# Kernel optimization log

Hardware: AMD Instinct MI355X
Metric: run time of the kernel (lower is better)

Reference implementation:

```python
import jax, jax.numpy as jnp
import numpy as np

E = 1024      # embed_dim
WS = 64       # window_size
B = 4
S = WS * WS   # residual add only works if seq_len == window_size**2
HID = 4 * E
EPS = 1e-5
SCALE = E ** -0.5


def _layer_norm(x, g, b):
    m = jnp.mean(x, axis=-1, keepdims=True)
    v = jnp.mean(jnp.square(x - m), axis=-1, keepdims=True)
    return (x - m) * jax.lax.rsqrt(v + EPS) * g + b


def setup_inputs() -> dict:
    key = jax.random.key(0)
    ks = jax.random.split(key, 12)
    std = 0.02
    return {
        "x":  jax.random.normal(ks[0], (B, S, E), jnp.float32),
        "Wq": jax.random.normal(ks[1], (E, E), jnp.float32) * std,
        "bq": jnp.zeros((E,), jnp.float32),
        "Wk": jax.random.normal(ks[2], (E, E), jnp.float32) * std,
        "bk": jnp.zeros((E,), jnp.float32),
        "Wv": jax.random.normal(ks[3], (E, E), jnp.float32) * std,
        "bv": jnp.zeros((E,), jnp.float32),
        "g1": jnp.ones((E,), jnp.float32),
        "be1": jnp.zeros((E,), jnp.float32),
        "W1": jax.random.normal(ks[4], (E, HID), jnp.float32) * std,
        "b1": jnp.zeros((HID,), jnp.float32),
        "W2": jax.random.normal(ks[5], (HID, E), jnp.float32) * std,
        "b2": jnp.zeros((E,), jnp.float32),
        "g2": jnp.ones((E,), jnp.float32),
        "be2": jnp.zeros((E,), jnp.float32),
    }


def reference(x, Wq, bq, Wk, bk, Wv, bv, g1, be1, W1, b1, W2, b2, g2, be2):
    b, s, e = x.shape
    n = (b * s) // (WS * WS)
    q = (x @ Wq + bq).reshape(n, WS, WS, e)
    k = (x @ Wk + bk).reshape(n, WS, WS, e)
    v = (x @ Wv + bv).reshape(n, WS, WS, e)
    # per-window attention over the last WS tokens of each (n, w) group
    scores = jnp.einsum('nwqe,nwke->nwqk', q, k) * SCALE  # (n, WS, WS, WS)
    attn = jax.nn.softmax(scores, axis=-1)
    out = jnp.einsum('nwqk,nwke->nwqe', attn, v).reshape(b, s, e)
    x = _layer_norm(x + out, g1, be1)               # dropout is identity (eval)
    ffn = jax.nn.relu(x @ W1 + b1) @ W2 + b2
    x = _layer_norm(x + ffn, g2, be2)
    return x
```

## Files before the change

### kernel.cpp

```cpp
#include <hip/hip_runtime.h>
#include <hip/hip_bf16.h>
#include <stdint.h>


typedef __attribute__((ext_vector_type(4))) float f32x4;
typedef __attribute__((ext_vector_type(8))) short bf16x8;
typedef __attribute__((ext_vector_type(4))) short bf16x4;

__device__ __forceinline__ void async_cp16(const void* g, void* l) {
    __builtin_amdgcn_global_load_lds(
        (const __attribute__((address_space(1))) void*)g,
        (__attribute__((address_space(3))) void*)l,
        16, 0, 0);
}

__device__ __forceinline__ short f2bf(float f) {
    __hip_bfloat16 h = __float2bfloat16(f);
    return __builtin_bit_cast(short, h);
}
__device__ __forceinline__ float bf2f(short s) {
    return __bfloat162float(__builtin_bit_cast(__hip_bfloat16, s));
}

template <int RELU, int MODE>
__global__ __launch_bounds__(512, 2) void gemm256_kernel(
    const short* __restrict__ A, int lda,
    const short* __restrict__ Bt, int ldb,
    const float* __restrict__ bias,
    void* __restrict__ Cv, int ldc,
    int M, int N, int K)
{
    __shared__ __align__(16) short lds[65536];

    const int t = threadIdx.x;
    const int wave = t >> 6, lane = t & 63;
    const int quad = lane >> 4, l16 = lane & 15;
    const int wm = wave >> 2, wn = wave & 3;
    const long m0 = (long)blockIdx.x * 256;
    const long n0 = (long)blockIdx.y * 256;

    const int srow = t >> 2;
    const int sg = t & 3;
    const int lr0 = srow ^ ((srow >> 2) & 1);
    const int lg0 = sg ^ (lr0 & 3);
    const short* gA = A + (m0 + lr0) * (long)lda + lg0 * 8;
    const short* gB = Bt + (n0 + lr0) * (long)ldb + lg0 * 8;
    const int wdst = wave * 512;

    int offA[8], offB[4];
#pragma unroll
    for (int mf = 0; mf < 8; ++mf) {
        const int row = wm * 128 + mf * 16 + l16;
        offA[mf] = (row * 32 + quad * 8) ^ ((row & 7) << 3);
    }
#pragma unroll
    for (int nf = 0; nf < 4; ++nf) {
        const int row = wn * 64 + nf * 16 + l16;
        offB[nf] = (row * 32 + quad * 8) ^ ((row & 7) << 3);
    }

    f32x4 acc[8][4] = {};
    const int NT = K >> 6;

#define STAGE_A(ksub, kt, buf)                                                 \
    do {                                                                       \
        const int ko_ = (kt) * 64 + (ksub) * 32;                               \
        short* d_ = lds + (buf) * 32768 + (ksub) * 8192 + wdst;                \
        async_cp16(gA + ko_, d_);                                              \
        async_cp16(gA + 128 * (long)lda + ko_, d_ + 4096);                     \
    } while (0)
#define STAGE_B(ksub, kt, buf)                                                 \
    do {                                                                       \
        const int ko_ = (kt) * 64 + (ksub) * 32;                               \
        short* d_ = lds + (buf) * 32768 + 16384 + (ksub) * 8192 + wdst;        \
        async_cp16(gB + ko_, d_);                                              \
        async_cp16(gB + 128 * (long)ldb + ko_, d_ + 4096);                     \
    } while (0)

    STAGE_A(0, 0, 0); STAGE_B(0, 0, 0); STAGE_A(1, 0, 0); STAGE_B(1, 0, 0);
    asm volatile("s_waitcnt vmcnt(4)" ::: "memory");
    __builtin_amdgcn_s_barrier();

    for (int kt = 0; kt < NT; ++kt) {
        const int cbuf = kt & 1, nbuf = cbuf ^ 1;
        const short* Ab = lds + cbuf * 32768;
        const short* Bb = Ab + 16384;
        const bool more = (kt + 1 < NT);

        bf16x8 av[4], bv[4];

#pragma unroll
        for (int nf = 0; nf < 4; ++nf) bv[nf] = *(const bf16x8*)(Bb + offB[nf]);
#pragma unroll
        for (int i = 0; i < 4; ++i) av[i] = *(const bf16x8*)(Ab + offA[i]);
        if (more) STAGE_A(0, kt + 1, nbuf);
        __builtin_amdgcn_s_barrier();
        asm volatile("s_waitcnt lgkmcnt(0)" ::: "memory");
        __builtin_amdgcn_sched_barrier(0);
        __builtin_amdgcn_s_setprio(1);
#pragma unroll
        for (int i = 0; i < 4; ++i)
#pragma unroll
            for (int nf = 0; nf < 4; ++nf)
                acc[i][nf] = __builtin_amdgcn_mfma_f32_16x16x32_bf16(
                    av[i], bv[nf], acc[i][nf], 0, 0, 0);
        __builtin_amdgcn_s_setprio(0);
        __builtin_amdgcn_s_barrier();

#pragma unroll
        for (int i = 0; i < 4; ++i) av[i] = *(const bf16x8*)(Ab + offA[4 + i]);
        if (more) STAGE_B(0, kt + 1, nbuf);
        __builtin_amdgcn_s_barrier();
        asm volatile("s_waitcnt lgkmcnt(0)" ::: "memory");
        __builtin_amdgcn_sched_barrier(0);
        __builtin_amdgcn_s_setprio(1);
#pragma unroll
        for (int i = 0; i < 4; ++i)
#pragma unroll
            for (int nf = 0; nf < 4; ++nf)
                acc[4 + i][nf] = __builtin_amdgcn_mfma_f32_16x16x32_bf16(
                    av[i], bv[nf], acc[4 + i][nf], 0, 0, 0);
        __builtin_amdgcn_s_setprio(0);
        if (more) asm volatile("s_waitcnt vmcnt(4)" ::: "memory");
        else      asm volatile("s_waitcnt vmcnt(0)" ::: "memory");
        __builtin_amdgcn_s_barrier();

#pragma unroll
        for (int nf = 0; nf < 4; ++nf) bv[nf] = *(const bf16x8*)(Bb + 8192 + offB[nf]);
#pragma unroll
        for (int i = 0; i < 4; ++i) av[i] = *(const bf16x8*)(Ab + 8192 + offA[i]);
        if (more) STAGE_A(1, kt + 1, nbuf);
        __builtin_amdgcn_s_barrier();
        asm volatile("s_waitcnt lgkmcnt(0)" ::: "memory");
        __builtin_amdgcn_sched_barrier(0);
        __builtin_amdgcn_s_setprio(1);
#pragma unroll
        for (int i = 0; i < 4; ++i)
#pragma unroll
            for (int nf = 0; nf < 4; ++nf)
                acc[i][nf] = __builtin_amdgcn_mfma_f32_16x16x32_bf16(
                    av[i], bv[nf], acc[i][nf], 0, 0, 0);
        __builtin_amdgcn_s_setprio(0);
        __builtin_amdgcn_s_barrier();

#pragma unroll
        for (int i = 0; i < 4; ++i) av[i] = *(const bf16x8*)(Ab + 8192 + offA[4 + i]);
        if (more) STAGE_B(1, kt + 1, nbuf);
        __builtin_amdgcn_s_barrier();
        asm volatile("s_waitcnt lgkmcnt(0)" ::: "memory");
        __builtin_amdgcn_sched_barrier(0);
        __builtin_amdgcn_s_setprio(1);
#pragma unroll
        for (int i = 0; i < 4; ++i)
#pragma unroll
            for (int nf = 0; nf < 4; ++nf)
                acc[4 + i][nf] = __builtin_amdgcn_mfma_f32_16x16x32_bf16(
                    av[i], bv[nf], acc[4 + i][nf], 0, 0, 0);
        __builtin_amdgcn_s_setprio(0);
        if (more) {
            asm volatile("s_waitcnt vmcnt(4)" ::: "memory");
            __builtin_amdgcn_s_barrier();
        }
    }
#undef STAGE_A
#undef STAGE_B

#pragma unroll
    for (int mf = 0; mf < 8; ++mf) {
#pragma unroll
        for (int nf = 0; nf < 4; ++nf) {
            const int n = (int)n0 + wn * 64 + nf * 16 + l16;
            const float bz = (MODE == 2) ? 0.f : bias[n];
#pragma unroll
            for (int r = 0; r < 4; ++r) {
                const long m = m0 + wm * 128 + mf * 16 + quad * 4 + r;
                float v = acc[mf][nf][r] + bz;
                if (MODE == 0) {
                    if (RELU) v = fmaxf(v, 0.f);
                    ((short*)Cv)[m * ldc + n] = f2bf(v);
                } else if (MODE == 1) {
                    ((float*)Cv)[m * ldc + n] = v;
                } else {
                    ((float*)Cv)[m * ldc + n] += v;
                }
            }
        }
    }
}

__global__ __launch_bounds__(256) void attn_mfma_kernel(
    const short* __restrict__ QKV, short* __restrict__ O)
{
    __shared__ __align__(16) float Sf[64 * 65];
    __shared__ __align__(16) short Pb[64 * 72];
    __shared__ __align__(16) short Vt[256 * 72];

    const int t = threadIdx.x;
    const int wave = t >> 6, lane = t & 63;
    const int quad = lane >> 4, l16 = lane & 15;
    const long rowbase = (long)blockIdx.x * 64;
    const short* Qg = QKV + rowbase * 3072;
    const short* Kg = Qg + 1024;
    const short* Vg = Qg + 2048;

    {
        const int wy = wave >> 1, wx = wave & 1;
        const short* qp0 = Qg + (long)(wy * 32 + l16) * 3072 + quad * 8;
        const short* qp1 = qp0 + 16 * 3072;
        const short* kp0 = Kg + (long)(wx * 32 + l16) * 3072 + quad * 8;
        const short* kp1 = kp0 + 16 * 3072;

        f32x4 s00 = {}, s01 = {}, s10 = {}, s11 = {};
        bf16x8 a0 = *(const bf16x8*)qp0;
        bf16x8 a1 = *(const bf16x8*)qp1;
        bf16x8 b0 = *(const bf16x8*)kp0;
        bf16x8 b1 = *(const bf16x8*)kp1;

#pragma unroll 2
        for (int k0 = 0; k0 < 1024; k0 += 32) {
            const int kn = (k0 + 32 < 1024) ? k0 + 32 : 0;
            bf16x8 na0 = *(const bf16x8*)(qp0 + kn);
            bf16x8 na1 = *(const bf16x8*)(qp1 + kn);
            bf16x8 nb0 = *(const bf16x8*)(kp0 + kn);
            bf16x8 nb1 = *(const bf16x8*)(kp1 + kn);
            s00 = __builtin_amdgcn_mfma_f32_16x16x32_bf16(a0, b0, s00, 0, 0, 0);
            s01 = __builtin_amdgcn_mfma_f32_16x16x32_bf16(a0, b1, s01, 0, 0, 0);
            s10 = __builtin_amdgcn_mfma_f32_16x16x32_bf16(a1, b0, s10, 0, 0, 0);
            s11 = __builtin_amdgcn_mfma_f32_16x16x32_bf16(a1, b1, s11, 0, 0, 0);
            a0 = na0; a1 = na1; b0 = nb0; b1 = nb1;
        }

        const int rb = wy * 32 + quad * 4;
        const int cb = wx * 32 + l16;
#pragma unroll
        for (int r = 0; r < 4; ++r) {
            Sf[(rb + r) * 65 + cb]           = s00[r] * 0.03125f;
            Sf[(rb + r) * 65 + cb + 16]      = s01[r] * 0.03125f;
            Sf[(rb + 16 + r) * 65 + cb]      = s10[r] * 0.03125f;
            Sf[(rb + 16 + r) * 65 + cb + 16] = s11[r] * 0.03125f;
        }
    }
    __syncthreads();

    {
        const int row = t >> 2;
        const int cs = (t & 3) * 16;
        const float* sp = Sf + row * 65 + cs;
        float v[16];
        float mx = -1e30f;
#pragma unroll
        for (int j = 0; j < 16; ++j) { v[j] = sp[j]; mx = fmaxf(mx, v[j]); }
        mx = fmaxf(mx, __shfl_xor(mx, 1, 64));
        mx = fmaxf(mx, __shfl_xor(mx, 2, 64));
        float sum = 0.f;
#pragma unroll
        for (int j = 0; j < 16; ++j) { v[j] = __expf(v[j] - mx); sum += v[j]; }
        sum += __shfl_xor(sum, 1, 64);
        sum += __shfl_xor(sum, 2, 64);
        const float inv = 1.f / sum;
        short* pp = Pb + row * 72 + cs;
        bf16x8 o0, o1;
#pragma unroll
        for (int j = 0; j < 8; ++j) { o0[j] = f2bf(v[j] * inv); o1[j] = f2bf(v[8 + j] * inv); }
        *(bf16x8*)(pp) = o0;
        *(bf16x8*)(pp + 8) = o1;
    }
    __syncthreads();

    bf16x8 am[2][4];
#pragma unroll
    for (int ki = 0; ki < 2; ++ki)
#pragma unroll
        for (int mi = 0; mi < 4; ++mi)
            am[ki][mi] = *(const bf16x8*)(Pb + (mi * 16 + l16) * 72 + ki * 32 + quad * 8);

    for (int nc = 0; nc < 4; ++nc) {
        const int nbase = nc * 256;
#pragma unroll
        for (int it = 0; it < 8; ++it) {
            const int idx = it * 256 + t;
            const int tok = idx >> 5;
            const int grp = idx & 31;
            bf16x8 v = *(const bf16x8*)(Vg + (long)tok * 3072 + nbase + grp * 8);
            const int tsw = tok ^ ((grp & 7) << 3);
            short* dst = Vt + (grp * 8) * 72 + tsw;
#pragma unroll
            for (int j = 0; j < 8; ++j) dst[j * 72] = v[j];
        }
        __syncthreads();

        f32x4 acc[4][4] = {};
#pragma unroll
        for (int ki = 0; ki < 2; ++ki) {
            bf16x8 bn[4];
#pragma unroll
            for (int ni = 0; ni < 4; ++ni) {
                const int e_local = wave * 64 + ni * 16 + l16;
                const int s = (e_local >> 3) & 7;
                bn[ni] = *(const bf16x8*)(Vt + e_local * 72 + ((ki * 32 + quad * 8) ^ (s << 3)));
            }
#pragma unroll
            for (int mi = 0; mi < 4; ++mi)
#pragma unroll
                for (int ni = 0; ni < 4; ++ni)
                    acc[mi][ni] = __builtin_amdgcn_mfma_f32_16x16x32_bf16(
                        am[ki][mi], bn[ni], acc[mi][ni], 0, 0, 0);
        }

#pragma unroll
        for (int mi = 0; mi < 4; ++mi)
#pragma unroll
            for (int ni = 0; ni < 4; ++ni) {
                const long n = nbase + wave * 64 + ni * 16 + l16;
#pragma unroll
                for (int r = 0; r < 4; ++r) {
                    const long m = rowbase + mi * 16 + quad * 4 + r;
                    O[m * 1024 + n] = f2bf(acc[mi][ni][r]);
                }
            }
        __syncthreads();
    }
}

__global__ __launch_bounds__(256, 4) void ln1_kernel(
    const float* __restrict__ X, const short* __restrict__ R,
    const float* __restrict__ gamma, const float* __restrict__ beta,
    short* __restrict__ Y)
{
    __shared__ float red[8];
    const int t = threadIdx.x;
    const int wave = t >> 6, lane = t & 63;
    const long row = blockIdx.x;

    f32x4 xv = *(const f32x4*)(X + row * 1024 + t * 4);
    bf16x4 rv = *(const bf16x4*)(R + row * 1024 + t * 4);
    float v[4];
    float s = 0.f, sq = 0.f;
#pragma unroll
    for (int i = 0; i < 4; ++i) {
        v[i] = xv[i] + bf2f(rv[i]);
        s += v[i];
        sq += v[i] * v[i];
    }
#pragma unroll
    for (int off = 32; off > 0; off >>= 1) {
        s  += __shfl_down(s, off, 64);
        sq += __shfl_down(sq, off, 64);
    }
    if (lane == 0) { red[wave] = s; red[4 + wave] = sq; }
    __syncthreads();
    if (t == 0) {
        float S = red[0] + red[1] + red[2] + red[3];
        float Q = red[4] + red[5] + red[6] + red[7];
        float mean = S * (1.f / 1024.f);
        float var = fmaxf(Q * (1.f / 1024.f) - mean * mean, 0.f);
        red[0] = mean;
        red[1] = rsqrtf(var + 1e-5f);
    }
    __syncthreads();
    const float mean = red[0], rstd = red[1];
    f32x4 gv = *(const f32x4*)(gamma + t * 4);
    f32x4 bv = *(const f32x4*)(beta + t * 4);
    bf16x4 yv;
#pragma unroll
    for (int i = 0; i < 4; ++i)
        yv[i] = f2bf((v[i] - mean) * rstd * gv[i] + bv[i]);
    *(bf16x4*)(Y + row * 1024 + t * 4) = yv;
}

__global__ __launch_bounds__(256, 4) void ln2_kernel(
    const short* __restrict__ X1, float* __restrict__ F,
    const float* __restrict__ gamma, const float* __restrict__ beta)
{
    __shared__ float red[8];
    const int t = threadIdx.x;
    const int wave = t >> 6, lane = t & 63;
    const long row = blockIdx.x;

    bf16x4 xv = *(const bf16x4*)(X1 + row * 1024 + t * 4);
    f32x4 fv = *(const f32x4*)(F + row * 1024 + t * 4);
    float v[4];
    float s = 0.f, sq = 0.f;
#pragma unroll
    for (int i = 0; i < 4; ++i) {
        v[i] = bf2f(xv[i]) + fv[i];
        s += v[i];
        sq += v[i] * v[i];
    }
#pragma unroll
    for (int off = 32; off > 0; off >>= 1) {
        s  += __shfl_down(s, off, 64);
        sq += __shfl_down(sq, off, 64);
    }
    if (lane == 0) { red[wave] = s; red[4 + wave] = sq; }
    __syncthreads();
    if (t == 0) {
        float S = red[0] + red[1] + red[2] + red[3];
        float Q = red[4] + red[5] + red[6] + red[7];
        float mean = S * (1.f / 1024.f);
        float var = fmaxf(Q * (1.f / 1024.f) - mean * mean, 0.f);
        red[0] = mean;
        red[1] = rsqrtf(var + 1e-5f);
    }
    __syncthreads();
    const float mean = red[0], rstd = red[1];
    f32x4 gv = *(const f32x4*)(gamma + t * 4);
    f32x4 bv = *(const f32x4*)(beta + t * 4);
    f32x4 yv;
#pragma unroll
    for (int i = 0; i < 4; ++i)
        yv[i] = (v[i] - mean) * rstd * gv[i] + bv[i];
    *(f32x4*)(F + row * 1024 + t * 4) = yv;
}

__global__ __launch_bounds__(256, 2) void transpose_kernel(
    const float* __restrict__ W, short* __restrict__ WT, int K, int N)
{
    __shared__ __align__(16) short tile[64 * 72];
    const int t = threadIdx.x;
    const long kb = (long)blockIdx.x * 64, nb = (long)blockIdx.y * 64;
    const int r = t >> 3, c = (t & 7) << 3;
#pragma unroll
    for (int i = 0; i < 2; ++i) {
        f32x4 v0 = *(const f32x4*)(W + (kb + r + i * 32) * N + nb + c);
        f32x4 v1 = *(const f32x4*)(W + (kb + r + i * 32) * N + nb + c + 4);
        short* dst = tile + (r + i * 32) * 72 + c;
#pragma unroll
        for (int j = 0; j < 4; ++j) { dst[j] = f2bf(v0[j]); dst[4 + j] = f2bf(v1[j]); }
    }
    __syncthreads();
#pragma unroll
    for (int i = 0; i < 2; ++i) {
        const int rr = r + i * 32;
        bf16x8 o;
#pragma unroll
        for (int j = 0; j < 8; ++j) o[j] = tile[(c + j) * 72 + rr];
        *(bf16x8*)(WT + (nb + rr) * K + kb + c) = o;
    }
}

__global__ __launch_bounds__(256, 4) void cvt_kernel(
    const float* __restrict__ X, short* __restrict__ Y)
{
    const long i = ((long)blockIdx.x * 256 + threadIdx.x) * 4;
    f32x4 v = *(const f32x4*)(X + i);
    bf16x4 o;
#pragma unroll
    for (int j = 0; j < 4; ++j) o[j] = f2bf(v[j]);
    *(bf16x4*)(Y + i) = o;
}

__global__ void concat_bias_kernel(const float* __restrict__ bq,
                                   const float* __restrict__ bk,
                                   const float* __restrict__ bv,
                                   float* __restrict__ out)
{
    const int i = blockIdx.x * 256 + threadIdx.x;
    float v;
    if (i < 1024)      v = bq[i];
    else if (i < 2048) v = bk[i - 1024];
    else               v = bv[i - 2048];
    out[i] = v;
}

extern "C" void kernel_launch(void* const* d_in, const int* in_sizes, int n_in,
                              void* d_out, int out_size, void* d_ws, size_t ws_size,
                              hipStream_t stream)
{
    const float* x   = (const float*)d_in[0];
    const float* Wq  = (const float*)d_in[1];
    const float* bq  = (const float*)d_in[2];
    const float* Wk  = (const float*)d_in[3];
    const float* bk  = (const float*)d_in[4];
    const float* Wv  = (const float*)d_in[5];
    const float* bv  = (const float*)d_in[6];
    const float* g1  = (const float*)d_in[7];
    const float* be1 = (const float*)d_in[8];
    const float* W1  = (const float*)d_in[9];
    const float* b1  = (const float*)d_in[10];
    const float* W2  = (const float*)d_in[11];
    const float* b2  = (const float*)d_in[12];
    const float* g2  = (const float*)d_in[13];
    const float* be2 = (const float*)d_in[14];

    const int M = in_sizes[0] / 1024;
    float* F    = (float*)d_out;
    short* xbf  = (short*)d_out;
    short* Obf  = (short*)d_out + (size_t)M * 1024;

    char* ws = (char*)d_ws;
    short* WqkvT = (short*)ws;
    short* W1T   = (short*)(ws + 6291456);
    short* W2T   = (short*)(ws + 14680064);
    float* bqkv  = (float*)(ws + 23068672);
    short* QKV   = (short*)(ws + 23080960);
    short* Hh    = (short*)(ws + 23080960);
    short* x1    = (short*)(ws + 23080960 + (size_t)M * 2048 * 2);

    dim3 blk(256);
    dim3 blk5(512);
    transpose_kernel<<<dim3(16, 16), blk, 0, stream>>>(Wq, WqkvT,               1024, 1024);
    transpose_kernel<<<dim3(16, 16), blk, 0, stream>>>(Wk, WqkvT + 1024 * 1024, 1024, 1024);
    transpose_kernel<<<dim3(16, 16), blk, 0, stream>>>(Wv, WqkvT + 2048 * 1024, 1024, 1024);
    transpose_kernel<<<dim3(16, 64), blk, 0, stream>>>(W1, W1T, 1024, 4096);
    transpose_kernel<<<dim3(64, 16), blk, 0, stream>>>(W2, W2T, 4096, 1024);
    concat_bias_kernel<<<12, blk, 0, stream>>>(bq, bk, bv, bqkv);
    cvt_kernel<<<M, blk, 0, stream>>>(x, xbf);

    gemm256_kernel<0, 0><<<dim3(M / 256, 12), blk5, 0, stream>>>(
        xbf, 1024, WqkvT, 1024, bqkv, QKV, 3072, M, 3072, 1024);
    attn_mfma_kernel<<<M / 64, blk, 0, stream>>>(QKV, Obf);
    ln1_kernel<<<M, blk, 0, stream>>>(x, Obf, g1, be1, x1);
    gemm256_kernel<1, 0><<<dim3(M / 256, 8), blk5, 0, stream>>>(
        x1, 1024, W1T, 1024, b1, Hh, 2048, M, 2048, 1024);
    gemm256_kernel<0, 1><<<dim3(M / 256, 4), blk5, 0, stream>>>(
        Hh, 2048, W2T, 4096, b2, F, 1024, M, 1024, 2048);
    gemm256_kernel<1, 0><<<dim3(M / 256, 8), blk5, 0, stream>>>(
        x1, 1024, W1T + 2048 * 1024, 1024, b1 + 2048, Hh, 2048, M, 2048, 1024);
    gemm256_kernel<0, 2><<<dim3(M / 256, 4), blk5, 0, stream>>>(
        Hh, 2048, W2T + 2048, 4096, b2, F, 1024, M, 1024, 2048);
    ln2_kernel<<<M, blk, 0, stream>>>(x1, F, g2, be2);
}
```

Baseline: 676.0 us.

## Restructure GEMM main loop into register-prefetched quadrant MFMA schedule

Reorganizes the 256x256 GEMM K-loop. All four global->LDS copies for the next tile are issued at the start of each iteration, and the loop now works over quadrants of the output (A rows 0-3/4-7 crossed with B cols low/high) with both k-subtiles per quadrant. Fragments for the next tile are loaded from LDS into registers before the last MFMA block runs, and partial lgkmcnt waits let LDS reads overlap MFMA execution. The aim is fewer barriers and waits per k-step and more LDS-latency hiding, at the cost of many more live registers (A0/A4/Bl/Bh), which may lower occupancy or cause spills.

```diff
diff --git a/kernel.cpp b/kernel.cpp
--- a/kernel.cpp
+++ b/kernel.cpp
@@ -77,9 +77,23 @@
         async_cp16(gB + 128 * (long)ldb + ko_, d_ + 4096);                     \
     } while (0)
 
+    bf16x8 A0[8], A4[8], Bl[4], Bh[4];
+
     STAGE_A(0, 0, 0); STAGE_B(0, 0, 0); STAGE_A(1, 0, 0); STAGE_B(1, 0, 0);
-    asm volatile("s_waitcnt vmcnt(4)" ::: "memory");
+    asm volatile("s_waitcnt vmcnt(0)" ::: "memory");
     __builtin_amdgcn_s_barrier();
+    {
+        const short* Ab = lds;
+        const short* Bb = lds + 16384;
+#pragma unroll
+        for (int i = 0; i < 4; ++i) A0[i]     = *(const bf16x8*)(Ab + offA[i]);
+#pragma unroll
+        for (int i = 0; i < 4; ++i) A0[4 + i] = *(const bf16x8*)(Ab + 8192 + offA[i]);
+        Bl[0] = *(const bf16x8*)(Bb + offB[0]);
+        Bl[1] = *(const bf16x8*)(Bb + offB[1]);
+        Bl[2] = *(const bf16x8*)(Bb + 8192 + offB[0]);
+        Bl[3] = *(const bf16x8*)(Bb + 8192 + offB[1]);
+    }
 
     for (int kt = 0; kt < NT; ++kt) {
         const int cbuf = kt & 1, nbuf = cbuf ^ 1;
@@ -87,80 +101,85 @@
         const short* Bb = Ab + 16384;
         const bool more = (kt + 1 < NT);
 
-        bf16x8 av[4], bv[4];
-
-#pragma unroll
-        for (int nf = 0; nf < 4; ++nf) bv[nf] = *(const bf16x8*)(Bb + offB[nf]);
-#pragma unroll
-        for (int i = 0; i < 4; ++i) av[i] = *(const bf16x8*)(Ab + offA[i]);
-        if (more) STAGE_A(0, kt + 1, nbuf);
+        if (more) {
+            STAGE_A(0, kt + 1, nbuf); STAGE_B(0, kt + 1, nbuf);
+            STAGE_A(1, kt + 1, nbuf); STAGE_B(1, kt + 1, nbuf);
+        }
+
+        Bh[0] = *(const bf16x8*)(Bb + offB[2]);
+        Bh[1] = *(const bf16x8*)(Bb + offB[3]);
+        Bh[2] = *(const bf16x8*)(Bb + 8192 + offB[2]);
+        Bh[3] = *(const bf16x8*)(Bb + 8192 + offB[3]);
+        asm volatile("s_waitcnt lgkmcnt(4)" ::: "memory");
+        __builtin_amdgcn_sched_barrier(0);
+        __builtin_amdgcn_s_setprio(1);
+#pragma unroll
+        for (int ks = 0; ks < 2; ++ks)
+#pragma unroll
+            for (int mf = 0; mf < 4; ++mf)
+#pragma unroll
+                for (int nf = 0; nf < 2; ++nf)
+                    acc[mf][nf] = __builtin_amdgcn_mfma_f32_16x16x32_bf16(
+                        A0[ks * 4 + mf], Bl[ks * 2 + nf], acc[mf][nf], 0, 0, 0);
+        __builtin_amdgcn_s_setprio(0);
         __builtin_amdgcn_s_barrier();
+
+#pragma unroll
+        for (int i = 0; i < 4; ++i) A4[i]     = *(const bf16x8*)(Ab + offA[4 + i]);
+#pragma unroll
+        for (int i = 0; i < 4; ++i) A4[4 + i] = *(const bf16x8*)(Ab + 8192 + offA[4 + i]);
+        asm volatile("s_waitcnt lgkmcnt(8)" ::: "memory");
+        __builtin_amdgcn_sched_barrier(0);
+        __builtin_amdgcn_s_setprio(1);
+#pragma unroll
+        for (int ks = 0; ks < 2; ++ks)
+#pragma unroll
+            for (int mf = 0; mf < 4; ++mf)
+#pragma unroll
+                for (int nf = 0; nf < 2; ++nf)
+                    acc[mf][2 + nf] = __builtin_amdgcn_mfma_f32_16x16x32_bf16(
+                        A0[ks * 4 + mf], Bh[ks * 2 + nf], acc[mf][2 + nf], 0, 0, 0);
+        __builtin_amdgcn_s_setprio(0);
+        __builtin_amdgcn_s_barrier();
+
         asm volatile("s_waitcnt lgkmcnt(0)" ::: "memory");
         __builtin_amdgcn_sched_barrier(0);
         __builtin_amdgcn_s_setprio(1);
 #pragma unroll
-        for (int i = 0; i < 4; ++i)
-#pragma unroll
-            for (int nf = 0; nf < 4; ++nf)
-                acc[i][nf] = __builtin_amdgcn_mfma_f32_16x16x32_bf16(
-                    av[i], bv[nf], acc[i][nf], 0, 0, 0);
+        for (int ks = 0; ks < 2; ++ks)
+#pragma unroll
+            for (int mf = 0; mf < 4; ++mf)
+#pragma unroll
+                for (int nf = 0; nf < 2; ++nf)
+                    acc[4 + mf][nf] = __builtin_amdgcn_mfma_f32_16x16x32_bf16(
+                        A4[ks * 4 + mf], Bl[ks * 2 + nf], acc[4 + mf][nf], 0, 0, 0);
+        __builtin_amdgcn_s_setprio(0);
+        if (more) asm volatile("s_waitcnt vmcnt(0)" ::: "memory");
+        __builtin_amdgcn_s_barrier();
+
+        if (more) {
+            const short* nA = lds + nbuf * 32768;
+            const short* nB = nA + 16384;
+#pragma unroll
+            for (int i = 0; i < 4; ++i) A0[i]     = *(const bf16x8*)(nA + offA[i]);
+#pragma unroll
+            for (int i = 0; i < 4; ++i) A0[4 + i] = *(const bf16x8*)(nA + 8192 + offA[i]);
+            Bl[0] = *(const bf16x8*)(nB + offB[0]);
+            Bl[1] = *(const bf16x8*)(nB + offB[1]);
+            Bl[2] = *(const bf16x8*)(nB + 8192 + offB[0]);
+            Bl[3] = *(const bf16x8*)(nB + 8192 + offB[1]);
+        }
+        __builtin_amdgcn_s_setprio(1);
+#pragma unroll
+        for (int ks = 0; ks < 2; ++ks)
+#pragma unroll
+            for (int mf = 0; mf < 4; ++mf)
+#pragma unroll
+                for (int nf = 0; nf < 2; ++nf)
+                    acc[4 + mf][2 + nf] = __builtin_amdgcn_mfma_f32_16x16x32_bf16(
+                        A4[ks * 4 + mf], Bh[ks * 2 + nf], acc[4 + mf][2 + nf], 0, 0, 0);
         __builtin_amdgcn_s_setprio(0);
         __builtin_amdgcn_s_barrier();
-
-#pragma unroll
-        for (int i = 0; i < 4; ++i) av[i] = *(const bf16x8*)(Ab + offA[4 + i]);
-        if (more) STAGE_B(0, kt + 1, nbuf);
-        __builtin_amdgcn_s_barrier();
-        asm volatile("s_waitcnt lgkmcnt(0)" ::: "memory");
-        __builtin_amdgcn_sched_barrier(0);
-        __builtin_amdgcn_s_setprio(1);
-#pragma unroll
-        for (int i = 0; i < 4; ++i)
-#pragma unroll
-            for (int nf = 0; nf < 4; ++nf)
-                acc[4 + i][nf] = __builtin_amdgcn_mfma_f32_16x16x32_bf16(
-                    av[i], bv[nf], acc[4 + i][nf], 0, 0, 0);
-        __builtin_amdgcn_s_setprio(0);
-        if (more) asm volatile("s_waitcnt vmcnt(4)" ::: "memory");
-        else      asm volatile("s_waitcnt vmcnt(0)" ::: "memory");
-        __builtin_amdgcn_s_barrier();
-
-#pragma unroll
-        for (int nf = 0; nf < 4; ++nf) bv[nf] = *(const bf16x8*)(Bb + 8192 + offB[nf]);
-#pragma unroll
-        for (int i = 0; i < 4; ++i) av[i] = *(const bf16x8*)(Ab + 8192 + offA[i]);
-        if (more) STAGE_A(1, kt + 1, nbuf);
-        __builtin_amdgcn_s_barrier();
-        asm volatile("s_waitcnt lgkmcnt(0)" ::: "memory");
-        __builtin_amdgcn_sched_barrier(0);
-        __builtin_amdgcn_s_setprio(1);
-#pragma unroll
-        for (int i = 0; i < 4; ++i)
-#pragma unroll
-            for (int nf = 0; nf < 4; ++nf)
-                acc[i][nf] = __builtin_amdgcn_mfma_f32_16x16x32_bf16(
-                    av[i], bv[nf], acc[i][nf], 0, 0, 0);
-        __builtin_amdgcn_s_setprio(0);
-        __builtin_amdgcn_s_barrier();
-
-#pragma unroll
-        for (int i = 0; i < 4; ++i) av[i] = *(const bf16x8*)(Ab + 8192 + offA[4 + i]);
-        if (more) STAGE_B(1, kt + 1, nbuf);
-        __builtin_amdgcn_s_barrier();
-        asm volatile("s_waitcnt lgkmcnt(0)" ::: "memory");
-        __builtin_amdgcn_sched_barrier(0);
-        __builtin_amdgcn_s_setprio(1);
-#pragma unroll
-        for (int i = 0; i < 4; ++i)
-#pragma unroll
-            for (int nf = 0; nf < 4; ++nf)
-                acc[4 + i][nf] = __builtin_amdgcn_mfma_f32_16x16x32_bf16(
-                    av[i], bv[nf], acc[4 + i][nf], 0, 0, 0);
-        __builtin_amdgcn_s_setprio(0);
-        if (more) {
-            asm volatile("s_waitcnt vmcnt(4)" ::: "memory");
-            __builtin_amdgcn_s_barrier();
-        }
     }
 #undef STAGE_A
 #undef STAGE_B
```

Result: slower. 718.7 us (+6.3%).
